# Kernel tuning notes

Measured on AMD Instinct MI355X. Metric: run time of the kernel, lower is better.

Reference implementation:

```python
import jax, jax.numpy as jnp
import numpy as np

# ---- equation / net constants (mirrors eqn_config / net_config) ----
NT = 256
DT = 0.04
N_HIST = 64
HIDDEN = 512
LAMBD = 1.0
MU1 = 0.08
MU2 = 0.02
R = 0.02
SIGMA = 0.2
BETA = 0.1
ETA = 0.5
LOGEPS = 1e-6
UTIL_PENALTY = 100.0
GEOMETRIC_SUM = (1.0 - np.exp(-LAMBD * DT * (N_HIST - 1))) / LAMBD  # discounted weight on oldest point
FINAL_DISC = float(np.exp(-BETA * NT * DT))


def setup_inputs() -> dict:
    key = jax.random.key(0)
    k = jax.random.split(key, 9)
    B = 16384
    dw_sample = jax.random.normal(k[0], (B, NT), dtype=jnp.float32) * np.sqrt(DT)
    x_init = jax.random.uniform(k[1], (B, N_HIST), dtype=jnp.float32) + 0.5  # positive initial wealth path
    # exponential kernel over the delay window (most recent point has weight ~1)
    exp_array = jnp.exp(-LAMBD * DT * jnp.arange(N_HIST - 1, 0, -1, dtype=jnp.float32))
    s1 = 1.0 / np.sqrt(N_HIST)
    s2 = 1.0 / np.sqrt(HIDDEN)
    W1 = jax.random.normal(k[2], (N_HIST, HIDDEN), dtype=jnp.float32) * s1
    b1 = jnp.zeros((HIDDEN,), dtype=jnp.float32)
    W2 = jax.random.normal(k[3], (HIDDEN, HIDDEN), dtype=jnp.float32) * s2
    b2 = jnp.zeros((HIDDEN,), dtype=jnp.float32)
    W3 = jax.random.normal(k[4], (HIDDEN, 2), dtype=jnp.float32) * s2
    b3 = jnp.zeros((2,), dtype=jnp.float32)
    return {"dw_sample": dw_sample, "x_init": x_init, "exp_array": exp_array,
            "W1": W1, "b1": b1, "W2": W2, "b2": b2, "W3": W3, "b3": b3}


def reference(dw_sample, x_init, exp_array, W1, b1, W2, b2, W3, b3):
    def util(v):  # log-utility with floor (util_tf)
        return jnp.log(jax.nn.relu(v) + LOGEPS)

    def policy(x_hist):  # feedforward policy on the history window; final_pi_tf = 2*sigmoid
        h = jax.nn.relu(x_hist @ W1 + b1)
        h = jax.nn.relu(h @ W2 + b2)
        return 2.0 * jax.nn.sigmoid(h @ W3 + b3)  # [B, 2]

    x = x_init[:, -1]                       # [B]
    x_hist0 = x_init                        # [B, N_HIST]
    y0 = jnp.sum(exp_array * x_init[:, 1:], axis=-1) * DT + GEOMETRIC_SUM * x_init[:, 0]
    reward0 = jnp.zeros_like(x)

    discounts = jnp.exp(-BETA * DT * jnp.arange(NT, dtype=jnp.float32))  # exp(-beta*t*dt)

    def step(carry, inputs):
        x, y, x_hist, reward = carry
        dw_t, disc = inputs                 # dw_t: [B], disc: scalar
        pi = policy(x_hist)                 # [B, 2]
        inst_r = util(pi[:, 0] * x) * disc - jax.nn.relu(-x) * UTIL_PENALTY
        reward = reward + inst_r * DT
        dx = ((MU1 - R) * pi[:, 1] - pi[:, 0] + R) * x + MU2 * y
        x_new = x + dx * DT + SIGMA * x * pi[:, 1] * dw_t
        y_new = y * jnp.exp(-DT * LAMBD) + x_new * DT
        x_hist_new = jnp.concatenate([x_hist[:, 1:], x_new[:, None]], axis=-1)
        return (x_new, y_new, x_hist_new, reward), None

    (x, y, _, reward), _ = jax.lax.scan(
        step, (x, y0, x_hist0, reward0), (dw_sample.T, discounts))

    # terminal step t == nt
    reward = reward + util(x + ETA * y) / BETA * FINAL_DISC
    reward = reward - jax.nn.relu(-x) * UTIL_PENALTY
    return -reward
```

## Files before the change

kernel.cpp:

```cpp
#include <hip/hip_runtime.h>
#include <stdint.h>
#include <stddef.h>

#define NTS 256

typedef short bf16x8 __attribute__((ext_vector_type(8)));
typedef short bf16x4 __attribute__((ext_vector_type(4)));
typedef float f32x4 __attribute__((ext_vector_type(4)));
typedef float f32x2 __attribute__((ext_vector_type(2)));
typedef unsigned int u32x2 __attribute__((ext_vector_type(2)));

__device__ __forceinline__ unsigned short f2bf(float f) {
  union { float f; unsigned u; } c; c.f = f;
  unsigned u = c.u;
  u += 0x7fffu + ((u >> 16) & 1u);
  return (unsigned short)(u >> 16);
}

__device__ __forceinline__ unsigned cvt_pk_bf16(float lo, float hi) {
  unsigned r;
  asm("v_cvt_pk_bf16_f32 %0, %1, %2" : "=v"(r) : "v"(lo), "v"(hi));
  return r;
}

__global__ __launch_bounds__(256) void prep_weights(const float* __restrict__ W1,
                                                    const float* __restrict__ W2,
                                                    unsigned short* __restrict__ wp) {
  int gid = blockIdx.x * 256 + threadIdx.x;
  if (gid >= 294912) return;
  int e = gid & 7, lane = (gid >> 3) & 63, fb = (gid >> 9) & 31, pan = gid >> 14;
  int q = lane >> 4, j = lane & 15, f = fb * 16 + j;
  float v;
  if (pan < 2) v = W1[(pan * 32 + q * 8 + e) * 512 + f];
  else         v = W2[((pan - 2) * 32 + q * 8 + e) * 512 + f];
  wp[gid] = f2bf(v);
}

__device__ __forceinline__ void stage_panel(const unsigned short* __restrict__ wp,
                                            int pan, char* dst_base, int wv, int lane) {
#pragma unroll
  for (int i = 0; i < 4; ++i) {
    const unsigned short* g = wp + (size_t)pan * 16384 + (wv * 4 + i) * 512 + lane * 8;
    char* l = dst_base + wv * 4096 + i * 1024;
    __builtin_amdgcn_global_load_lds((const __attribute__((address_space(1))) void*)g,
                                     (__attribute__((address_space(3))) void*)l,
                                     16, 0, 0);
  }
}

__global__ __launch_bounds__(512, 2) void po_fused(
    const float* __restrict__ dw, const float* __restrict__ x_init,
    const float* __restrict__ exp_arr, const float* __restrict__ b1,
    const float* __restrict__ b2, const float* __restrict__ W3,
    const float* __restrict__ b3, const unsigned short* __restrict__ wp,
    float* __restrict__ out) {
  extern __shared__ char smem[];
  char* const w1L = smem;
  char* const h1C = smem + 65536;
  char* const histC = smem + 131072;
  unsigned int* const h0L = (unsigned int*)(smem + 139264);
  float* const p0L = (float*)(smem + 143360);
  float* const p1L = (float*)(smem + 145408);
  float* const dwL = (float*)(smem + 147456);
  float* const b1L = (float*)(smem + 151552);
  float* const b2L = (float*)(smem + 153600);
  float* const w3L = (float*)(smem + 155648);

  const int tid = threadIdx.x;
  const int lane = tid & 63;
  const int wv = tid >> 6;
  const int q = lane >> 4;
  const int j = lane & 15;
  const int wg = blockIdx.x;

  b1L[tid] = b1[tid];
  b2L[tid] = b2[tid];
  w3L[tid] = W3[tid];
  w3L[tid + 512] = W3[tid + 512];

  const int b_h = (wv & 3) * 16 + j;
  {
    const int k0 = (wv >> 2) * 32 + q * 8;
    const float* src = x_init + ((size_t)wg * 64 + b_h) * 64 + k0;
    bf16x8 v;
#pragma unroll
    for (int e = 0; e < 8; ++e) v[e] = (short)f2bf(src[e]);
    *(bf16x8*)(histC + tid * 16) = v;
    h0L[tid] = (unsigned int)(unsigned short)v[0];
  }

  float xreg, yreg, rreg = 0.f;
  {
    const float* row = x_init + ((size_t)wg * 64 + lane) * 64;
    float y0 = 0.f;
    for (int k = 0; k < 63; ++k) y0 += exp_arr[k] * row[1 + k];
    yreg = y0 * 0.04f + (1.f - __expf(-2.52f)) * row[0];
    xreg = row[63];
  }
  const float b30 = b3[0], b31 = b3[1];

  stage_panel(wp, 0, w1L, wv, lane);
  stage_panel(wp, 1, w1L + 32768, wv, lane);

  const unsigned short* const wpW2 = wp + 32768;
  const int wfo = wv * 2048 + lane * 8;

  bf16x8 w0[4], w1r[4], w2r[4], w3r[4];
#pragma unroll
  for (int mt = 0; mt < 4; ++mt) {
    w0[mt]  = *(const bf16x8*)(wpW2 + 0 * 16384 + wfo + mt * 512);
    w1r[mt] = *(const bf16x8*)(wpW2 + 1 * 16384 + wfo + mt * 512);
    w2r[mt] = *(const bf16x8*)(wpW2 + 2 * 16384 + wfo + mt * 512);
    w3r[mt] = *(const bf16x8*)(wpW2 + 3 * 16384 + wfo + mt * 512);
  }

  __syncthreads();

  f32x4 acc[4][4];

  auto w2_phase = [&](bf16x8 (&wreg)[4], const char* h1b,
                      const unsigned short* wsrc) {
    bf16x8 bfr[4];
#pragma unroll
    for (int nt = 0; nt < 4; ++nt)
      bfr[nt] = *(const bf16x8*)(h1b + nt * 1024 + lane * 16);
    __builtin_amdgcn_s_setprio(1);
#pragma unroll
    for (int nt = 0; nt < 4; ++nt)
#pragma unroll
      for (int mt = 0; mt < 4; ++mt)
        acc[mt][nt] = __builtin_amdgcn_mfma_f32_16x16x32_bf16(wreg[mt], bfr[nt],
                                                              acc[mt][nt], 0, 0, 0);
    __builtin_amdgcn_s_setprio(0);
#pragma unroll
    for (int mt = 0; mt < 4; ++mt)
      wreg[mt] = *(const bf16x8*)(wsrc + wfo + mt * 512);
  };

#pragma unroll 1
  for (int t = 0; t < NTS; ++t) {
    if ((t & 15) == 0) {
      int b = tid >> 3, c = tid & 7;
      f32x2 v = *(const f32x2*)(dw + ((size_t)wg * 64 + b) * NTS + t + c * 2);
      dwL[(c * 2) * 64 + b] = v[0];
      dwL[(c * 2 + 1) * 64 + b] = v[1];
    }

#pragma unroll
    for (int mt = 0; mt < 4; ++mt)
#pragma unroll
      for (int nt = 0; nt < 4; ++nt) acc[mt][nt] = (f32x4){0.f, 0.f, 0.f, 0.f};
#pragma unroll
    for (int p = 0; p < 2; ++p) {
      const char* pb = w1L + p * 32768 + wv * 4096;
      bf16x8 bfr[4];
#pragma unroll
      for (int nt = 0; nt < 4; ++nt)
        bfr[nt] = *(const bf16x8*)(histC + ((p * 4 + nt) * 64 + lane) * 16);
#pragma unroll
      for (int mt = 0; mt < 4; ++mt) {
        bf16x8 afr = *(const bf16x8*)(pb + mt * 1024 + lane * 16);
#pragma unroll
        for (int nt = 0; nt < 4; ++nt)
          acc[mt][nt] = __builtin_amdgcn_mfma_f32_16x16x32_bf16(afr, bfr[nt],
                                                                acc[mt][nt], 0, 0, 0);
      }
    }
#pragma unroll
    for (int mt = 0; mt < 4; ++mt) {
      int f0 = wv * 64 + mt * 16 + q * 4;
      f32x4 b1v = *(const f32x4*)(b1L + f0);
      int wb = ((f0 >> 5) * 256 + ((f0 >> 3) & 3) * 16 + j) * 16 + (f0 & 7) * 2;
#pragma unroll
      for (int nt = 0; nt < 4; ++nt) {
        float v0 = fmaxf(acc[mt][nt][0] + b1v[0], 0.f);
        float v1 = fmaxf(acc[mt][nt][1] + b1v[1], 0.f);
        float v2 = fmaxf(acc[mt][nt][2] + b1v[2], 0.f);
        float v3 = fmaxf(acc[mt][nt][3] + b1v[3], 0.f);
        u32x2 pk;
        pk[0] = cvt_pk_bf16(v0, v1);
        pk[1] = cvt_pk_bf16(v2, v3);
        *(u32x2*)(h1C + wb + nt * 1024) = pk;
      }
    }
    __syncthreads();

#pragma unroll
    for (int mt = 0; mt < 4; ++mt)
#pragma unroll
      for (int nt = 0; nt < 4; ++nt) acc[mt][nt] = (f32x4){0.f, 0.f, 0.f, 0.f};
    {
      const unsigned short* pb = wpW2;
      const char* h1p = h1C;
#pragma unroll 1
      for (int a = 0; a < 4; ++a) {
        const unsigned short* pn = (a == 3) ? wpW2 : (pb + 4 * 16384);
        w2_phase(w0,  h1p,         pn);
        w2_phase(w1r, h1p + 4096,  pn + 16384);
        w2_phase(w2r, h1p + 8192,  pn + 32768);
        w2_phase(w3r, h1p + 12288, pn + 49152);
        pb += 4 * 16384;
        h1p += 16384;
      }
    }

    {
      float p0a[4] = {0.f, 0.f, 0.f, 0.f};
      float p1a[4] = {0.f, 0.f, 0.f, 0.f};
#pragma unroll
      for (int mt = 0; mt < 4; ++mt) {
        int f0 = wv * 64 + mt * 16 + q * 4;
        f32x4 b2v = *(const f32x4*)(b2L + f0);
        f32x4 w3a = *(const f32x4*)(w3L + f0 * 2);
        f32x4 w3b = *(const f32x4*)(w3L + f0 * 2 + 4);
#pragma unroll
        for (int nt = 0; nt < 4; ++nt) {
          float v0 = fmaxf(acc[mt][nt][0] + b2v[0], 0.f);
          float v1 = fmaxf(acc[mt][nt][1] + b2v[1], 0.f);
          float v2 = fmaxf(acc[mt][nt][2] + b2v[2], 0.f);
          float v3 = fmaxf(acc[mt][nt][3] + b2v[3], 0.f);
          p0a[nt] += v0 * w3a[0] + v1 * w3a[2] + v2 * w3b[0] + v3 * w3b[2];
          p1a[nt] += v0 * w3a[1] + v1 * w3a[3] + v2 * w3b[1] + v3 * w3b[3];
        }
      }
#pragma unroll
      for (int nt = 0; nt < 4; ++nt) {
        p0a[nt] += __shfl_xor(p0a[nt], 16);
        p0a[nt] += __shfl_xor(p0a[nt], 32);
        p1a[nt] += __shfl_xor(p1a[nt], 16);
        p1a[nt] += __shfl_xor(p1a[nt], 32);
        if (q == 0) {
          int b = nt * 16 + j;
          p0L[wv * 64 + b] = p0a[nt];
          p1L[wv * 64 + b] = p1a[nt];
        }
      }
    }
    __syncthreads();

    float xn;
    {
      float z0 = b30, z1 = b31;
#pragma unroll
      for (int w = 0; w < 8; ++w) {
        z0 += p0L[w * 64 + lane];
        z1 += p1L[w * 64 + lane];
      }
      float pi0 = 2.f / (1.f + __expf(-z0));
      float pi1 = 2.f / (1.f + __expf(-z1));
      float x = xreg, y = yreg;
      float disc = __expf(-0.004f * (float)t);
      float rv = fmaxf(pi0 * x, 0.f) + 1e-6f;
      rreg += (__logf(rv) * disc - fmaxf(-x, 0.f) * 100.f) * 0.04f;
      float dwv = dwL[(t & 15) * 64 + lane];
      float dxv = (0.06f * pi1 - pi0 + 0.02f) * x + 0.02f * y;
      xn = x + dxv * 0.04f + 0.2f * x * pi1 * dwv;
      yreg = y * 0.960789439152323f + xn * 0.04f;
      xreg = xn;
    }

    {
      bf16x8 own = *(const bf16x8*)(histC + tid * 16);
      int e0 = (int)(unsigned short)own[0];
      int nbr = __shfl_down(e0, 16);
      float xb = __shfl(xn, b_h);
      unsigned short xbf = f2bf(xb);
      unsigned short last;
      if (q == 3) {
        last = (wv >= 4) ? xbf
                         : (unsigned short)h0L[(t & 1) * 512 + tid + 208];
      } else {
        last = (unsigned short)nbr;
      }
      bf16x8 nw;
#pragma unroll
      for (int e = 0; e < 7; ++e) nw[e] = own[e + 1];
      nw[7] = (short)last;
      *(bf16x8*)(histC + tid * 16) = nw;
      h0L[((t + 1) & 1) * 512 + tid] = (unsigned int)(unsigned short)nw[0];
    }
    __syncthreads();
  }

  if (tid < 64) {
    float rw = rreg + __logf(fmaxf(xreg + 0.5f * yreg, 0.f) + 1e-6f) * 10.f * __expf(-1.024f);
    rw -= fmaxf(-xreg, 0.f) * 100.f;
    out[(size_t)wg * 64 + tid] = -rw;
  }
}

extern "C" void kernel_launch(void* const* d_in, const int* in_sizes, int n_in,
                              void* d_out, int out_size, void* d_ws, size_t ws_size,
                              hipStream_t stream) {
  const float* dw      = (const float*)d_in[0];
  const float* x_init  = (const float*)d_in[1];
  const float* exp_arr = (const float*)d_in[2];
  const float* W1      = (const float*)d_in[3];
  const float* b1      = (const float*)d_in[4];
  const float* W2      = (const float*)d_in[5];
  const float* b2      = (const float*)d_in[6];
  const float* W3      = (const float*)d_in[7];
  const float* b3      = (const float*)d_in[8];
  unsigned short* wp = (unsigned short*)d_ws;
  float* out = (float*)d_out;

  (void)hipFuncSetAttribute((const void*)po_fused,
                            hipFuncAttributeMaxDynamicSharedMemorySize, 160 * 1024);

  prep_weights<<<1152, 256, 0, stream>>>(W1, W2, wp);
  po_fused<<<256, 512, 159744, stream>>>(dw, x_init, exp_arr, b1, b2, W3, b3, wp, out);
}
```

Baseline: 2.184 ms.

## Switch MFMA tiles from 16x16x32 to 32x32x16 with matching weight layout

Replaces the 16x16x32 bf16 MFMA tiling with 32x32x16 tiles in both layer-1 and layer-2 GEMMs. The weight prep kernel, LDS history layout, h1 write-back layout, W2 register streaming, output reduction and history shift are all reworked for the new fragment shapes. The aim is fewer MFMA instructions and fewer operand loads per step, plus fewer cross-lane shuffles in the reduction. The cost is a larger accumulator block per instruction and layout complexity that must stay consistent across stages.

```diff
diff --git a/kernel.cpp b/kernel.cpp
--- a/kernel.cpp
+++ b/kernel.cpp
@@ -5,9 +5,9 @@
 #define NTS 256
 
 typedef short bf16x8 __attribute__((ext_vector_type(8)));
-typedef short bf16x4 __attribute__((ext_vector_type(4)));
 typedef float f32x4 __attribute__((ext_vector_type(4)));
 typedef float f32x2 __attribute__((ext_vector_type(2)));
+typedef float f32x16 __attribute__((ext_vector_type(16)));
 typedef unsigned int u32x2 __attribute__((ext_vector_type(2)));
 
 __device__ __forceinline__ unsigned short f2bf(float f) {
@@ -28,24 +28,12 @@
                                                     unsigned short* __restrict__ wp) {
   int gid = blockIdx.x * 256 + threadIdx.x;
   if (gid >= 294912) return;
-  int e = gid & 7, lane = (gid >> 3) & 63, fb = (gid >> 9) & 31, pan = gid >> 14;
-  int q = lane >> 4, j = lane & 15, f = fb * 16 + j;
+  int e = gid & 7, lane = (gid >> 3) & 63, fb = (gid >> 9) & 15, pan = gid >> 13;
+  int k = (lane >> 5) * 8 + e, f = fb * 32 + (lane & 31);
   float v;
-  if (pan < 2) v = W1[(pan * 32 + q * 8 + e) * 512 + f];
-  else         v = W2[((pan - 2) * 32 + q * 8 + e) * 512 + f];
+  if (pan < 4) v = W1[(pan * 16 + k) * 512 + f];
+  else         v = W2[((pan - 4) * 16 + k) * 512 + f];
   wp[gid] = f2bf(v);
-}
-
-__device__ __forceinline__ void stage_panel(const unsigned short* __restrict__ wp,
-                                            int pan, char* dst_base, int wv, int lane) {
-#pragma unroll
-  for (int i = 0; i < 4; ++i) {
-    const unsigned short* g = wp + (size_t)pan * 16384 + (wv * 4 + i) * 512 + lane * 8;
-    char* l = dst_base + wv * 4096 + i * 1024;
-    __builtin_amdgcn_global_load_lds((const __attribute__((address_space(1))) void*)g,
-                                     (__attribute__((address_space(3))) void*)l,
-                                     16, 0, 0);
-  }
 }
 
 __global__ __launch_bounds__(512, 2) void po_fused(
@@ -69,8 +57,8 @@
   const int tid = threadIdx.x;
   const int lane = tid & 63;
   const int wv = tid >> 6;
-  const int q = lane >> 4;
-  const int j = lane & 15;
+  const int hi = lane >> 5;
+  const int cl = lane & 31;
   const int wg = blockIdx.x;
 
   b1L[tid] = b1[tid];
@@ -78,10 +66,10 @@
   w3L[tid] = W3[tid];
   w3L[tid + 512] = W3[tid + 512];
 
-  const int b_h = (wv & 3) * 16 + j;
+  const int b_col = (wv & 1) * 32 + cl;
   {
-    const int k0 = (wv >> 2) * 32 + q * 8;
-    const float* src = x_init + ((size_t)wg * 64 + b_h) * 64 + k0;
+    const int k0 = (wv >> 1) * 16 + hi * 8;
+    const float* src = x_init + ((size_t)wg * 64 + b_col) * 64 + k0;
     bf16x8 v;
 #pragma unroll
     for (int e = 0; e < 8; ++e) v[e] = (short)f2bf(src[e]);
@@ -99,42 +87,43 @@
   }
   const float b30 = b3[0], b31 = b3[1];
 
-  stage_panel(wp, 0, w1L, wv, lane);
-  stage_panel(wp, 1, w1L + 32768, wv, lane);
+#pragma unroll
+  for (int i = 0; i < 8; ++i) {
+    const unsigned short* g = wp + i * 4096 + wv * 512 + lane * 8;
+    char* l = w1L + i * 8192 + wv * 1024;
+    __builtin_amdgcn_global_load_lds((const __attribute__((address_space(1))) void*)g,
+                                     (__attribute__((address_space(3))) void*)l,
+                                     16, 0, 0);
+  }
 
   const unsigned short* const wpW2 = wp + 32768;
-  const int wfo = wv * 2048 + lane * 8;
-
-  bf16x8 w0[4], w1r[4], w2r[4], w3r[4];
-#pragma unroll
-  for (int mt = 0; mt < 4; ++mt) {
-    w0[mt]  = *(const bf16x8*)(wpW2 + 0 * 16384 + wfo + mt * 512);
-    w1r[mt] = *(const bf16x8*)(wpW2 + 1 * 16384 + wfo + mt * 512);
-    w2r[mt] = *(const bf16x8*)(wpW2 + 2 * 16384 + wfo + mt * 512);
-    w3r[mt] = *(const bf16x8*)(wpW2 + 3 * 16384 + wfo + mt * 512);
+  const int wfo = wv * 1024 + lane * 8;
+
+  bf16x8 w0[2], w1r[2], w2r[2], w3r[2];
+#pragma unroll
+  for (int mt = 0; mt < 2; ++mt) {
+    w0[mt]  = *(const bf16x8*)(wpW2 + 0 * 8192 + wfo + mt * 512);
+    w1r[mt] = *(const bf16x8*)(wpW2 + 1 * 8192 + wfo + mt * 512);
+    w2r[mt] = *(const bf16x8*)(wpW2 + 2 * 8192 + wfo + mt * 512);
+    w3r[mt] = *(const bf16x8*)(wpW2 + 3 * 8192 + wfo + mt * 512);
   }
 
   __syncthreads();
 
-  f32x4 acc[4][4];
-
-  auto w2_phase = [&](bf16x8 (&wreg)[4], const char* h1b,
+  f32x16 acc[2][2];
+
+  auto w2_phase = [&](bf16x8 (&wreg)[2], const char* h1b,
                       const unsigned short* wsrc) {
-    bf16x8 bfr[4];
-#pragma unroll
-    for (int nt = 0; nt < 4; ++nt)
-      bfr[nt] = *(const bf16x8*)(h1b + nt * 1024 + lane * 16);
+    bf16x8 bfr0 = *(const bf16x8*)(h1b + lane * 16);
+    bf16x8 bfr1 = *(const bf16x8*)(h1b + 1024 + lane * 16);
     __builtin_amdgcn_s_setprio(1);
-#pragma unroll
-    for (int nt = 0; nt < 4; ++nt)
-#pragma unroll
-      for (int mt = 0; mt < 4; ++mt)
-        acc[mt][nt] = __builtin_amdgcn_mfma_f32_16x16x32_bf16(wreg[mt], bfr[nt],
-                                                              acc[mt][nt], 0, 0, 0);
+    acc[0][0] = __builtin_amdgcn_mfma_f32_32x32x16_bf16(wreg[0], bfr0, acc[0][0], 0, 0, 0);
+    acc[0][1] = __builtin_amdgcn_mfma_f32_32x32x16_bf16(wreg[0], bfr1, acc[0][1], 0, 0, 0);
+    acc[1][0] = __builtin_amdgcn_mfma_f32_32x32x16_bf16(wreg[1], bfr0, acc[1][0], 0, 0, 0);
+    acc[1][1] = __builtin_amdgcn_mfma_f32_32x32x16_bf16(wreg[1], bfr1, acc[1][1], 0, 0, 0);
     __builtin_amdgcn_s_setprio(0);
-#pragma unroll
-    for (int mt = 0; mt < 4; ++mt)
-      wreg[mt] = *(const bf16x8*)(wsrc + wfo + mt * 512);
+    wreg[0] = *(const bf16x8*)(wsrc + wfo);
+    wreg[1] = *(const bf16x8*)(wsrc + wfo + 512);
   };
 
 #pragma unroll 1
@@ -147,92 +136,98 @@
     }
 
 #pragma unroll
-    for (int mt = 0; mt < 4; ++mt)
-#pragma unroll
-      for (int nt = 0; nt < 4; ++nt) acc[mt][nt] = (f32x4){0.f, 0.f, 0.f, 0.f};
-#pragma unroll
-    for (int p = 0; p < 2; ++p) {
-      const char* pb = w1L + p * 32768 + wv * 4096;
-      bf16x8 bfr[4];
-#pragma unroll
-      for (int nt = 0; nt < 4; ++nt)
-        bfr[nt] = *(const bf16x8*)(histC + ((p * 4 + nt) * 64 + lane) * 16);
-#pragma unroll
-      for (int mt = 0; mt < 4; ++mt) {
-        bf16x8 afr = *(const bf16x8*)(pb + mt * 1024 + lane * 16);
-#pragma unroll
-        for (int nt = 0; nt < 4; ++nt)
-          acc[mt][nt] = __builtin_amdgcn_mfma_f32_16x16x32_bf16(afr, bfr[nt],
+    for (int mt = 0; mt < 2; ++mt)
+#pragma unroll
+      for (int nt = 0; nt < 2; ++nt) acc[mt][nt] = (f32x16)(0.f);
+#pragma unroll
+    for (int p = 0; p < 4; ++p) {
+      bf16x8 bfr[2];
+#pragma unroll
+      for (int nt = 0; nt < 2; ++nt)
+        bfr[nt] = *(const bf16x8*)(histC + ((p * 2 + nt) * 64 + lane) * 16);
+#pragma unroll
+      for (int mt = 0; mt < 2; ++mt) {
+        bf16x8 afr = *(const bf16x8*)(w1L + ((p * 16 + wv * 2 + mt) * 64 + lane) * 16);
+#pragma unroll
+        for (int nt = 0; nt < 2; ++nt)
+          acc[mt][nt] = __builtin_amdgcn_mfma_f32_32x32x16_bf16(afr, bfr[nt],
                                                                 acc[mt][nt], 0, 0, 0);
       }
     }
 #pragma unroll
-    for (int mt = 0; mt < 4; ++mt) {
-      int f0 = wv * 64 + mt * 16 + q * 4;
-      f32x4 b1v = *(const f32x4*)(b1L + f0);
-      int wb = ((f0 >> 5) * 256 + ((f0 >> 3) & 3) * 16 + j) * 16 + (f0 & 7) * 2;
-#pragma unroll
-      for (int nt = 0; nt < 4; ++nt) {
-        float v0 = fmaxf(acc[mt][nt][0] + b1v[0], 0.f);
-        float v1 = fmaxf(acc[mt][nt][1] + b1v[1], 0.f);
-        float v2 = fmaxf(acc[mt][nt][2] + b1v[2], 0.f);
-        float v3 = fmaxf(acc[mt][nt][3] + b1v[3], 0.f);
-        u32x2 pk;
-        pk[0] = cvt_pk_bf16(v0, v1);
-        pk[1] = cvt_pk_bf16(v2, v3);
-        *(u32x2*)(h1C + wb + nt * 1024) = pk;
+    for (int mt = 0; mt < 2; ++mt) {
+      int fbase = (wv * 2 + mt) * 32 + 4 * hi;
+#pragma unroll
+      for (int r2 = 0; r2 < 4; ++r2) {
+        int f0 = fbase + 8 * r2;
+        f32x4 b1v = *(const f32x4*)(b1L + f0);
+        int ks = (wv * 2 + mt) * 2 + (r2 >> 1);
+        int lanep = cl + 32 * (r2 & 1);
+        char* dst = h1C + ((ks * 2) * 64 + lanep) * 16 + hi * 8;
+#pragma unroll
+        for (int nt = 0; nt < 2; ++nt) {
+          float v0 = fmaxf(acc[mt][nt][4 * r2 + 0] + b1v[0], 0.f);
+          float v1 = fmaxf(acc[mt][nt][4 * r2 + 1] + b1v[1], 0.f);
+          float v2 = fmaxf(acc[mt][nt][4 * r2 + 2] + b1v[2], 0.f);
+          float v3 = fmaxf(acc[mt][nt][4 * r2 + 3] + b1v[3], 0.f);
+          u32x2 pk;
+          pk[0] = cvt_pk_bf16(v0, v1);
+          pk[1] = cvt_pk_bf16(v2, v3);
+          *(u32x2*)(dst + nt * 1024) = pk;
+        }
       }
     }
     __syncthreads();
 
 #pragma unroll
-    for (int mt = 0; mt < 4; ++mt)
-#pragma unroll
-      for (int nt = 0; nt < 4; ++nt) acc[mt][nt] = (f32x4){0.f, 0.f, 0.f, 0.f};
+    for (int mt = 0; mt < 2; ++mt)
+#pragma unroll
+      for (int nt = 0; nt < 2; ++nt) acc[mt][nt] = (f32x16)(0.f);
     {
       const unsigned short* pb = wpW2;
       const char* h1p = h1C;
 #pragma unroll 1
-      for (int a = 0; a < 4; ++a) {
-        const unsigned short* pn = (a == 3) ? wpW2 : (pb + 4 * 16384);
-        w2_phase(w0,  h1p,         pn);
-        w2_phase(w1r, h1p + 4096,  pn + 16384);
-        w2_phase(w2r, h1p + 8192,  pn + 32768);
-        w2_phase(w3r, h1p + 12288, pn + 49152);
-        pb += 4 * 16384;
-        h1p += 16384;
+      for (int a = 0; a < 8; ++a) {
+        const unsigned short* pn = (a == 7) ? wpW2 : (pb + 4 * 8192);
+        w2_phase(w0,  h1p,        pn);
+        w2_phase(w1r, h1p + 2048, pn + 8192);
+        w2_phase(w2r, h1p + 4096, pn + 16384);
+        w2_phase(w3r, h1p + 6144, pn + 24576);
+        pb += 4 * 8192;
+        h1p += 8192;
       }
     }
 
     {
-      float p0a[4] = {0.f, 0.f, 0.f, 0.f};
-      float p1a[4] = {0.f, 0.f, 0.f, 0.f};
-#pragma unroll
-      for (int mt = 0; mt < 4; ++mt) {
-        int f0 = wv * 64 + mt * 16 + q * 4;
-        f32x4 b2v = *(const f32x4*)(b2L + f0);
-        f32x4 w3a = *(const f32x4*)(w3L + f0 * 2);
-        f32x4 w3b = *(const f32x4*)(w3L + f0 * 2 + 4);
-#pragma unroll
-        for (int nt = 0; nt < 4; ++nt) {
-          float v0 = fmaxf(acc[mt][nt][0] + b2v[0], 0.f);
-          float v1 = fmaxf(acc[mt][nt][1] + b2v[1], 0.f);
-          float v2 = fmaxf(acc[mt][nt][2] + b2v[2], 0.f);
-          float v3 = fmaxf(acc[mt][nt][3] + b2v[3], 0.f);
-          p0a[nt] += v0 * w3a[0] + v1 * w3a[2] + v2 * w3b[0] + v3 * w3b[2];
-          p1a[nt] += v0 * w3a[1] + v1 * w3a[3] + v2 * w3b[1] + v3 * w3b[3];
+      float p0a[2] = {0.f, 0.f};
+      float p1a[2] = {0.f, 0.f};
+#pragma unroll
+      for (int mt = 0; mt < 2; ++mt) {
+        int fbase = (wv * 2 + mt) * 32 + 4 * hi;
+#pragma unroll
+        for (int r2 = 0; r2 < 4; ++r2) {
+          int f0 = fbase + 8 * r2;
+          f32x4 b2v = *(const f32x4*)(b2L + f0);
+          f32x4 w3a = *(const f32x4*)(w3L + f0 * 2);
+          f32x4 w3b = *(const f32x4*)(w3L + f0 * 2 + 4);
+#pragma unroll
+          for (int nt = 0; nt < 2; ++nt) {
+            float v0 = fmaxf(acc[mt][nt][4 * r2 + 0] + b2v[0], 0.f);
+            float v1 = fmaxf(acc[mt][nt][4 * r2 + 1] + b2v[1], 0.f);
+            float v2 = fmaxf(acc[mt][nt][4 * r2 + 2] + b2v[2], 0.f);
+            float v3 = fmaxf(acc[mt][nt][4 * r2 + 3] + b2v[3], 0.f);
+            p0a[nt] += v0 * w3a[0] + v1 * w3a[2] + v2 * w3b[0] + v3 * w3b[2];
+            p1a[nt] += v0 * w3a[1] + v1 * w3a[3] + v2 * w3b[1] + v3 * w3b[3];
+          }
         }
       }
 #pragma unroll
-      for (int nt = 0; nt < 4; ++nt) {
-        p0a[nt] += __shfl_xor(p0a[nt], 16);
+      for (int nt = 0; nt < 2; ++nt) {
         p0a[nt] += __shfl_xor(p0a[nt], 32);
-        p1a[nt] += __shfl_xor(p1a[nt], 16);
         p1a[nt] += __shfl_xor(p1a[nt], 32);
-        if (q == 0) {
-          int b = nt * 16 + j;
-          p0L[wv * 64 + b] = p0a[nt];
-          p1L[wv * 64 + b] = p1a[nt];
+        if (hi == 0) {
+          p0L[wv * 64 + nt * 32 + cl] = p0a[nt];
+          p1L[wv * 64 + nt * 32 + cl] = p1a[nt];
         }
       }
     }
@@ -262,13 +257,13 @@
     {
       bf16x8 own = *(const bf16x8*)(histC + tid * 16);
       int e0 = (int)(unsigned short)own[0];
-      int nbr = __shfl_down(e0, 16);
-      float xb = __shfl(xn, b_h);
+      int nbr = __shfl_down(e0, 32);
+      float xb = __shfl(xn, b_col);
       unsigned short xbf = f2bf(xb);
       unsigned short last;
-      if (q == 3) {
-        last = (wv >= 4) ? xbf
-                         : (unsigned short)h0L[(t & 1) * 512 + tid + 208];
+      if (hi == 1) {
+        last = (wv >= 6) ? xbf
+                         : (unsigned short)h0L[(t & 1) * 512 + (wv + 2) * 64 + cl];
       } else {
         last = (unsigned short)nbr;
       }
```

After: 2.340 ms. 1.07x slower.
